# Kernel optimization log

Measured on AMD Instinct MI355X. Metric: run time of the kernel, lower is better.

Reference implementation:

```python
import jax, jax.numpy as jnp
import numpy as np

N, E, D, H, G = 40000, 640000, 128, 8, 64
DH = D // H
CUT = 8.0
LN2 = float(np.log(2.0))


def ssp(v):  # shifted softplus (SchNet activation)
    return jax.nn.softplus(v) - jnp.asarray(LN2, v.dtype)


def setup_inputs() -> dict:
    key = jax.random.key(0)
    ks = jax.random.split(key, 20)
    def lin(k, fi, fo):
        k1, k2 = jax.random.split(k)
        s = 1.0 / np.sqrt(fi)
        return (jax.random.uniform(k1, (fi, fo), jnp.float32, -s, s),
                jax.random.uniform(k2, (fo,), jnp.float32, -s, s))
    W_lin, b_lin = lin(ks[0], G, D)
    W_r1, b_r1 = lin(ks[1], G, D)
    W_r2, b_r2 = lin(ks[2], D, D)
    Wq, bq = lin(ks[3], D, D)
    Wk, bk = lin(ks[4], D, D)
    Wv, bv = lin(ks[5], D, D)
    Wo, bo = lin(ks[6], D, D)
    return {
        "x": jax.random.normal(ks[7], (N, D), jnp.float32),
        "t": jax.random.normal(ks[8], (N, D), jnp.float32),
        "f_ij": jax.random.uniform(ks[9], (E, G), jnp.float32),
        "r_ij": jax.random.uniform(ks[10], (E,), jnp.float32, 0.0, CUT),
        "src": jax.random.randint(ks[11], (E,), 0, N, jnp.int32),
        "dst": jax.random.randint(ks[12], (E,), 0, N, jnp.int32),
        "W_lin": W_lin, "b_lin": b_lin,
        "W_r1": W_r1, "b_r1": b_r1, "W_r2": W_r2, "b_r2": b_r2,
        "Wq": Wq, "bq": bq, "Wk": Wk, "bk": bk, "Wv": Wv, "bv": bv,
        "Wo": Wo, "bo": bo,
        "ln_g": jnp.ones((D,), jnp.float32),
        "ln_b": jnp.zeros((D,), jnp.float32),
    }


def reference(x, t, f_ij, r_ij, src, dst,
              W_lin, b_lin, W_r1, b_r1, W_r2, b_r2,
              Wq, bq, Wk, bk, Wv, bv, Wo, bo, ln_g, ln_b):
    # filter-generating network: linear branch + resnet branch (resnet=True)
    W = f_ij @ W_lin + b_lin + (ssp(f_ij @ W_r1 + b_r1) @ W_r2 + b_r2)  # [E, D]
    # cosine cutoff
    C = 0.5 * (jnp.cos(jnp.pi * r_ij / CUT) + 1.0) * (r_ij < CUT)  # [E]
    W = W * C[:, None]
    # time-conditioned node representation
    h = x + t  # [N, D]
    # ego attention: queries from destination node, keys/values from filtered messages
    q = (h @ Wq + bq).reshape(N, H, DH)
    m = h[src] * W  # filtered neighbor messages [E, D]
    k = (m @ Wk + bk).reshape(E, H, DH)
    v = (m @ Wv + bv).reshape(E, H, DH)
    scores = jnp.einsum('ehd,ehd->eh', q[dst], k) / np.sqrt(DH)  # [E, H]
    # per-destination segment softmax
    smax = jax.ops.segment_max(scores, dst, num_segments=N)  # [N, H]
    ex = jnp.exp(scores - smax[dst])
    den = jax.ops.segment_sum(ex, dst, num_segments=N)
    alpha = ex / (den[dst] + 1e-16)  # [E, H]
    agg = jax.ops.segment_sum(alpha[:, :, None] * v, dst, num_segments=N)  # [N, H, DH]
    vout = agg.reshape(N, D) @ Wo + bo
    # residual + post layer norm
    out = x + vout
    mu = jnp.mean(out, axis=-1, keepdims=True)
    var = jnp.var(out, axis=-1, keepdims=True)
    out = (out - mu) / jnp.sqrt(var + 1e-5) * ln_g + ln_b
    return out
```

## Files before the change

### kernel.cpp

```cpp
#include <hip/hip_runtime.h>

#define NN 40000
#define EE 640000
#define DD 128
#define HH 8
#define GG 64

typedef unsigned short u16;
typedef __attribute__((ext_vector_type(8))) short short8;
typedef __attribute__((ext_vector_type(4))) float f32x4;

__device__ __forceinline__ float bf2f(u16 u){ union{unsigned i;float f;}v; v.i=((unsigned)u)<<16; return v.f; }
__device__ __forceinline__ u16 f2bf(float f){ union{float f;unsigned i;}v; v.f=f; unsigned r=v.i+0x7fffu+((v.i>>16)&1u); return (u16)(r>>16); }
__device__ __forceinline__ float ssp_fast(float x){
  float t=fminf(x*1.4426950408889634f,126.0f);
  float p=__builtin_amdgcn_exp2f(t);
  return 0.6931471805599453f*(__builtin_amdgcn_logf(1.0f+p)-1.0f);
}

__device__ __forceinline__ bool bfmode(const void* lng){ return *(const unsigned*)lng == 0x3F803F80u; }
__device__ __forceinline__ float ldf(const void* p, int i, bool bf){
  return bf ? bf2f(((const u16*)p)[i]) : ((const float*)p)[i];
}
__device__ __forceinline__ u16 ldb(const void* p, int i, bool bf){
  return bf ? ((const u16*)p)[i] : f2bf(((const float*)p)[i]);
}

#define MFMA16(a,b,c) __builtin_amdgcn_mfma_f32_16x16x32_bf16((a),(b),(c),0,0,0)
__device__ __forceinline__ short8 frag16(const u16* p){ return *(const short8*)p; }

#define DPPADD(x,ctrl) do{ union{float f;int i;}_a,_b; _a.f=(x); \
  _b.i=__builtin_amdgcn_update_dpp(0,_a.i,(ctrl),0xF,0xF,true); (x)+=_b.f; }while(0)
__device__ __forceinline__ float red16(float x){
  DPPADD(x,0xB1); DPPADD(x,0x4E); DPPADD(x,0x124); DPPADD(x,0x128);
  return x;
}

__device__ __forceinline__ void bar_lgkm(){
  asm volatile("s_waitcnt lgkmcnt(0)\n\ts_barrier" ::: "memory");
}

__global__ __launch_bounds__(512) void k1_hq(const void* __restrict__ x, const void* __restrict__ t,
        const void* __restrict__ Wq, const void* __restrict__ bq, const void* __restrict__ lng,
        u16* __restrict__ h_out, u16* __restrict__ q_out){
  extern __shared__ u16 s1[];
  u16* wq = s1;
  u16* hb = wq+16384;
  float* bqf=(float*)(hb+8704);
  bool bf=bfmode(lng);
  {
    int cc=threadIdx.x&127, kg0=threadIdx.x>>7;
    for (int kg=kg0; kg<16; kg+=4){
      uint4 u; u16* tp=(u16*)&u;
      #pragma unroll
      for (int j=0;j<8;j++) tp[j]=ldb(Wq,(kg*8+j)*128+cc,bf);
      *(uint4*)&wq[(kg*128+cc)*8]=u;
    }
    if (threadIdx.x<128) bqf[threadIdx.x]=ldf(bq,threadIdx.x,bf);
  }
  int wave=threadIdx.x>>6, lane=threadIdx.x&63;
  int mb=wave>>1, nh=wave&1, lrow=lane&15, quad=lane>>4;
  int r0=blockIdx.x*64;
  #pragma unroll
  for (int i=0;i<2;i++){
    int idx=threadIdx.x+i*512;
    int row=idx>>4, part=idx&15;
    size_t g=(size_t)(r0+row)*128+part*8;
    uint4 u; u16* tp=(u16*)&u;
    if (bf){
      uint4 xv=*(const uint4*)((const u16*)x+g);
      uint4 tv=*(const uint4*)((const u16*)t+g);
      const u16* xp=(const u16*)&xv; const u16* tq=(const u16*)&tv;
      #pragma unroll
      for (int j=0;j<8;j++) tp[j]=f2bf(bf2f(xp[j])+bf2f(tq[j]));
    } else {
      const float* xp=(const float*)x+g; const float* tq=(const float*)t+g;
      float4 a0=*(const float4*)xp, a1=*(const float4*)(xp+4);
      float4 b0=*(const float4*)tq, b1=*(const float4*)(tq+4);
      float va[8]={a0.x+b0.x,a0.y+b0.y,a0.z+b0.z,a0.w+b0.w,
                   a1.x+b1.x,a1.y+b1.y,a1.z+b1.z,a1.w+b1.w};
      #pragma unroll
      for (int j=0;j<8;j++) tp[j]=f2bf(va[j]);
    }
    *(uint4*)&h_out[g]=u;
    *(uint4*)&hb[row*136+part*8]=u;
  }
  __syncthreads();
  short8 ma[4];
  const u16* mr=&hb[(mb*16+lrow)*136];
  #pragma unroll
  for (int ks=0;ks<4;ks++) ma[ks]=frag16(&mr[ks*32+quad*8]);
  #pragma unroll
  for (int nb=0;nb<4;nb++){
    int col=nh*64+nb*16+lrow;
    f32x4 acc={0.f,0.f,0.f,0.f};
    #pragma unroll
    for (int ks=0;ks<4;ks++) acc=MFMA16(ma[ks], frag16(&wq[((ks*4+quad)*128+col)*8]), acc);
    float bb=bqf[col];
    #pragma unroll
    for (int r=0;r<4;r++)
      q_out[(size_t)(r0+mb*16+quad*4+r)*128+col]=f2bf(acc[r]+bb);
  }
}

__global__ __launch_bounds__(256) void k_hist(const int* __restrict__ dst, int* __restrict__ counts){
  int e=blockIdx.x*256+threadIdx.x;
  atomicAdd(&counts[dst[e]],1);
}

__global__ __launch_bounds__(1024) void k_scan(const int* __restrict__ counts, int* __restrict__ row_start){
  __shared__ int part[1024];
  int tid=threadIdx.x;
  const int CH=(NN+1023)/1024;
  int base=tid*CH, s=0;
  for (int i=0;i<CH;i++){ int idx=base+i; if (idx<NN) s+=counts[idx]; }
  part[tid]=s; __syncthreads();
  for (int off=1;off<1024;off<<=1){
    int v=(tid>=off)?part[tid-off]:0;
    __syncthreads();
    part[tid]+=v;
    __syncthreads();
  }
  int run=part[tid]-s;
  for (int i=0;i<CH;i++){ int idx=base+i; if (idx<NN){ row_start[idx]=run; run+=counts[idx]; } }
  if (tid==1023) row_start[NN]=part[1023];
}

__global__ __launch_bounds__(256) void k_scatter(const int* __restrict__ dst, const int* __restrict__ row_start,
    int* __restrict__ cursor, int* __restrict__ edge_list){
  int e=blockIdx.x*256+threadIdx.x;
  int d=dst[e];
  int pos=row_start[d]+atomicAdd(&cursor[d],1);
  edge_list[pos]=e;
}

__global__ __launch_bounds__(512) void e_fused(
    const void* __restrict__ f_ij, const void* __restrict__ r_ij,
    const int* __restrict__ src, const int* __restrict__ dst,
    const void* __restrict__ W_lin, const void* __restrict__ b_lin,
    const void* __restrict__ W_r1, const void* __restrict__ b_r1,
    const void* __restrict__ W_r2, const void* __restrict__ b_r2,
    const void* __restrict__ Wk, const void* __restrict__ bk,
    const void* __restrict__ Wv, const void* __restrict__ bv,
    const void* __restrict__ lng,
    const u16* __restrict__ h_g, const u16* __restrict__ q_g,
    float* __restrict__ scores_out, u16* __restrict__ v_out)
{
  extern __shared__ u16 sm[];
  u16* wr1   = sm;
  u16* wlin  = wr1 + 8192;
  u16* wr2   = wlin + 8192;
  u16* wk    = wr2 + 16384;
  u16* ov    = wk + 16384;
  u16* f_lds = ov;
  u16* t_lds = ov + 4608;
  u16* m_lds = ov + 4608 + 8704;
  float* br1 = (float*)(sm + 71168);
  float* bl2 = br1 + 128;
  float* bkf = bl2 + 128;
  float* bvf = bkf + 128;
  bool bf = bfmode(lng);

  {
    int c=threadIdx.x&127, kg0=threadIdx.x>>7;
    for (int kg=kg0; kg<8; kg+=4){
      uint4 u; u16* tp=(u16*)&u;
      #pragma unroll
      for (int j=0;j<8;j++) tp[j]=ldb(W_r1,(kg*8+j)*128+c,bf);
      *(uint4*)&wr1[(kg*128+c)*8]=u;
      #pragma unroll
      for (int j=0;j<8;j++) tp[j]=ldb(W_lin,(kg*8+j)*128+c,bf);
      *(uint4*)&wlin[(kg*128+c)*8]=u;
    }
    for (int kg=kg0; kg<16; kg+=4){
      uint4 u; u16* tp=(u16*)&u;
      #pragma unroll
      for (int j=0;j<8;j++) tp[j]=ldb(W_r2,(kg*8+j)*128+c,bf);
      *(uint4*)&wr2[(kg*128+c)*8]=u;
      #pragma unroll
      for (int j=0;j<8;j++) tp[j]=ldb(Wk,(kg*8+j)*128+c,bf);
      *(uint4*)&wk[(kg*128+c)*8]=u;
      #pragma unroll
      for (int j=0;j<8;j++) tp[j]=ldb(Wv,(kg*8+j)*128+c,bf);
      *(uint4*)&ov[(kg*128+c)*8]=u;
    }
    if (threadIdx.x<128){
      br1[threadIdx.x]=ldf(b_r1,threadIdx.x,bf);
      bl2[threadIdx.x]=ldf(b_lin,threadIdx.x,bf)+ldf(b_r2,threadIdx.x,bf);
      bkf[threadIdx.x]=ldf(bk,threadIdx.x,bf);
      bvf[threadIdx.x]=ldf(bv,threadIdx.x,bf);
    }
  }
  __syncthreads();

  int wave=threadIdx.x>>6, lane=threadIdx.x&63;
  int mb=wave>>1, nh=wave&1, lrow=lane&15, quad=lane>>4;
  int erow0=mb*16+quad*4;
  int fedge=threadIdx.x>>3, fpart=threadIdx.x&7;
  const int NT=EE/64;

  short8 wvf[16];
  #pragma unroll
  for (int nb=0;nb<4;nb++){
    int col=nh*64+nb*16+lrow;
    #pragma unroll
    for (int ks=0;ks<4;ks++)
      wvf[nb*4+ks]=frag16(&ov[((ks*4+quad)*128+col)*8]);
  }
  __syncthreads();

  float4 fA, fB;
  int4 sv, dv;
  float rr0,rr1,rr2,rr3;
  u16 hc[4][4], qc[4][4];
  u16 hn[4][4], qn[4][4];
  float cc[4];

  auto LOAD_F=[&](int tt){
    if (bf){
      fA = *(const float4*)((const u16*)f_ij + (size_t)(tt*64+fedge)*64 + fpart*8);
    } else {
      const float* fp=(const float*)f_ij + (size_t)(tt*64+fedge)*64 + fpart*8;
      fA = *(const float4*)fp;
      fB = *(const float4*)(fp+4);
    }
  };
  auto WRITE_F=[&](){
    uint4 u;
    if (bf) u=*(uint4*)&fA;
    else {
      u16* tp=(u16*)&u;
      const float* a=(const float*)&fA;
      const float* b=(const float*)&fB;
      #pragma unroll
      for (int j=0;j<4;j++){ tp[j]=f2bf(a[j]); tp[4+j]=f2bf(b[j]); }
    }
    *(uint4*)&f_lds[fedge*72+fpart*8]=u;
  };
  auto LOAD_SDR=[&](int tt){
    sv=*(const int4*)&src[tt*64+erow0];
    dv=*(const int4*)&dst[tt*64+erow0];
    rr0=ldf(r_ij,tt*64+erow0+0,bf);
    rr1=ldf(r_ij,tt*64+erow0+1,bf);
    rr2=ldf(r_ij,tt*64+erow0+2,bf);
    rr3=ldf(r_ij,tt*64+erow0+3,bf);
  };
  auto LOAD_HQ=[&](u16 (&hd)[4][4], u16 (&qd)[4][4]){
    int sa[4]={sv.x,sv.y,sv.z,sv.w};
    int da[4]={dv.x,dv.y,dv.z,dv.w};
    #pragma unroll
    for (int nb=0;nb<4;nb++){
      int col=nh*64+nb*16+lrow;
      #pragma unroll
      for (int r=0;r<4;r++){
        hd[nb][r]=h_g[(size_t)sa[r]*128+col];
        qd[nb][r]=q_g[(size_t)da[r]*128+col];
      }
    }
  };
  auto CUTOFF=[&](){
    float ra[4]={rr0,rr1,rr2,rr3};
    #pragma unroll
    for (int r=0;r<4;r++)
      cc[r]=(ra[r]<8.0f)?0.5f*(__cosf(ra[r]*0.39269908169872414f)+1.0f):0.0f;
  };

  int tile=blockIdx.x;
  {
    LOAD_F(tile); LOAD_SDR(tile);
    WRITE_F();
    LOAD_HQ(hc,qc);
    CUTOFF();
  }
  __syncthreads();

  for (; tile<NT; tile+=gridDim.x){
    int tn=tile+gridDim.x; if (tn>=NT) tn=tile;

    const u16* fr=&f_lds[(mb*16+lrow)*72];
    short8 a0=frag16(&fr[quad*8]);
    short8 a1=frag16(&fr[32+quad*8]);

    LOAD_F(tn);
    LOAD_SDR(tn);

    #pragma unroll
    for (int nb=0;nb<4;nb++){
      int col=nh*64+nb*16+lrow;
      f32x4 acc={0.f,0.f,0.f,0.f};
      acc=MFMA16(a0, frag16(&wr1[(quad*128+col)*8]), acc);
      acc=MFMA16(a1, frag16(&wr1[((4+quad)*128+col)*8]), acc);
      float bb=br1[col];
      #pragma unroll
      for (int r=0;r<4;r++){
        int er=mb*16+quad*4+r;
        t_lds[er*136+col]=f2bf(ssp_fast(acc[r]+bb));
      }
    }
    bar_lgkm();

    WRITE_F();
    LOAD_HQ(hn,qn);

    short8 ta[4];
    const u16* tr=&t_lds[(mb*16+lrow)*136];
    #pragma unroll
    for (int ks=0;ks<4;ks++) ta[ks]=frag16(&tr[ks*32+quad*8]);
    #pragma unroll
    for (int nb=0;nb<4;nb++){
      int col=nh*64+nb*16+lrow;
      f32x4 acc={0.f,0.f,0.f,0.f};
      acc=MFMA16(a0, frag16(&wlin[(quad*128+col)*8]), acc);
      acc=MFMA16(a1, frag16(&wlin[((4+quad)*128+col)*8]), acc);
      #pragma unroll
      for (int ks=0;ks<4;ks++)
        acc=MFMA16(ta[ks], frag16(&wr2[((ks*4+quad)*128+col)*8]), acc);
      float bb=bl2[col];
      #pragma unroll
      for (int r=0;r<4;r++){
        int er=mb*16+quad*4+r;
        float u=(acc[r]+bb)*cc[r];
        m_lds[er*136+col]=f2bf(u*bf2f(hc[nb][r]));
      }
    }
    bar_lgkm();

    short8 ma[4];
    const u16* mr=&m_lds[(mb*16+lrow)*136];
    #pragma unroll
    for (int ks=0;ks<4;ks++) ma[ks]=frag16(&mr[ks*32+quad*8]);

    #pragma unroll
    for (int nb=0;nb<4;nb++){
      int col=nh*64+nb*16+lrow;
      f32x4 acc={0.f,0.f,0.f,0.f};
      #pragma unroll
      for (int ks=0;ks<4;ks++) acc=MFMA16(ma[ks], frag16(&wk[((ks*4+quad)*128+col)*8]), acc);
      float bb=bkf[col];
      float p[4];
      #pragma unroll
      for (int r=0;r<4;r++)
        p[r]=(acc[r]+bb)*bf2f(qc[nb][r]);
      #pragma unroll
      for (int r=0;r<4;r++) p[r]=red16(p[r]);
      if (lrow==0){
        int head=nh*4+nb;
        #pragma unroll
        for (int r=0;r<4;r++){
          int er=mb*16+quad*4+r;
          scores_out[(size_t)(tile*64+er)*8+head]=p[r]*0.25f;
        }
      }
      f32x4 av={0.f,0.f,0.f,0.f};
      #pragma unroll
      for (int ks=0;ks<4;ks++) av=MFMA16(ma[ks], wvf[nb*4+ks], av);
      float bb2=bvf[col];
      #pragma unroll
      for (int r=0;r<4;r++){
        int er=mb*16+quad*4+r;
        v_out[(size_t)(tile*64+er)*128+col]=f2bf(av[r]+bb2);
      }
    }

    #pragma unroll
    for (int nb=0;nb<4;nb++){
      #pragma unroll
      for (int r=0;r<4;r++){ hc[nb][r]=hn[nb][r]; qc[nb][r]=qn[nb][r]; }
    }
    CUTOFF();
  }
}

__global__ __launch_bounds__(256) void k3a_agg(
    const int* __restrict__ row_start, const int* __restrict__ edge_list,
    const float* __restrict__ scores, const u16* __restrict__ v_g,
    u16* __restrict__ agg_out)
{
  __shared__ int   el_s[2][128];
  __shared__ float al_s[2][128*8];
  __shared__ float mxden[2][16];
  int half=threadIdx.x>>7, tid=threadIdx.x&127;
  int n=blockIdx.x*2+half;
  int s0=row_start[n], s1=row_start[n+1], deg=s1-s0;
  int dc=min(deg,128);
  if (tid<dc) el_s[half][tid]=edge_list[s0+tid];
  __syncthreads();
  int h=tid>>4, j=tid&15;
  float mr=-1e30f, sr=0.f;
  for (int p=j;p<deg;p+=16){
    int e=(p<128)?el_s[half][p]:edge_list[s0+p];
    float sc=scores[(size_t)e*8+h];
    float mn=fmaxf(mr,sc);
    sr=sr*__expf(mr-mn)+__expf(sc-mn);
    mr=mn;
  }
  #pragma unroll
  for (int off=1;off<16;off<<=1){
    float m2=__shfl_xor(mr,off,64), s2=__shfl_xor(sr,off,64);
    float mn=fmaxf(mr,m2);
    sr=sr*__expf(mr-mn)+s2*__expf(m2-mn);
    mr=mn;
  }
  if (j==0){ mxden[half][h]=mr; mxden[half][8+h]=1.0f/(sr+1e-16f); }
  __syncthreads();
  {
    float mx=mxden[half][h], rd=mxden[half][8+h];
    for (int p=j;p<dc;p+=16){
      int e=el_s[half][p];
      al_s[half][p*8+h]=__expf(scores[(size_t)e*8+h]-mx)*rd;
    }
  }
  __syncthreads();
  int c=tid, hc=c>>4;
  float mxc=mxden[half][hc], rdc=mxden[half][8+hc];
  float agg=0.f;
  int p=0;
  for (; p+4<=dc; p+=4){
    int e0=el_s[half][p],   e1=el_s[half][p+1];
    int e2=el_s[half][p+2], e3=el_s[half][p+3];
    float a0=al_s[half][p*8+hc],     a1=al_s[half][(p+1)*8+hc];
    float a2=al_s[half][(p+2)*8+hc], a3=al_s[half][(p+3)*8+hc];
    agg += a0*bf2f(v_g[(size_t)e0*128+c]);
    agg += a1*bf2f(v_g[(size_t)e1*128+c]);
    agg += a2*bf2f(v_g[(size_t)e2*128+c]);
    agg += a3*bf2f(v_g[(size_t)e3*128+c]);
  }
  for (; p<dc; p++)
    agg += al_s[half][p*8+hc]*bf2f(v_g[(size_t)el_s[half][p]*128+c]);
  for (; p<deg; p++){
    int e=edge_list[s0+p];
    agg += __expf(scores[(size_t)e*8+hc]-mxc)*rdc*bf2f(v_g[(size_t)e*128+c]);
  }
  agg_out[(size_t)n*128+c]=f2bf(agg);
}

__global__ __launch_bounds__(512) void k3b_out(
    const u16* __restrict__ agg_g, const void* __restrict__ x_g,
    const void* __restrict__ Wo, const void* __restrict__ bo,
    const void* __restrict__ lng, const void* __restrict__ lnb,
    void* __restrict__ out)
{
  extern __shared__ u16 smb[];
  u16* wo = smb;
  u16* ag = wo+16384;
  float* bof=(float*)(ag+64*136);
  float* lgf=bof+128;
  float* lbf=lgf+128;
  float* rsum=lbf+128;
  float* rsq =rsum+128;
  bool bf=bfmode(lng);
  {
    int cc=threadIdx.x&127, kg0=threadIdx.x>>7;
    for (int kg=kg0; kg<16; kg+=4){
      uint4 u; u16* tp=(u16*)&u;
      #pragma unroll
      for (int jj=0;jj<8;jj++) tp[jj]=ldb(Wo,(kg*8+jj)*128+cc,bf);
      *(uint4*)&wo[(kg*128+cc)*8]=u;
    }
    if (threadIdx.x<128){
      bof[threadIdx.x]=ldf(bo,threadIdx.x,bf);
      lgf[threadIdx.x]=ldf(lng,threadIdx.x,bf);
      lbf[threadIdx.x]=ldf(lnb,threadIdx.x,bf);
    }
  }
  int wave=threadIdx.x>>6, lane=threadIdx.x&63;
  int mb=wave>>1, nh=wave&1, lrow=lane&15, quad=lane>>4;
  for (int tile=blockIdx.x; tile<NN/64; tile+=gridDim.x){
    int r0=tile*64;
    #pragma unroll
    for (int i=0;i<2;i++){
      int idx=threadIdx.x+i*512;
      int row=idx>>4, part=idx&15;
      uint4 d=*(const uint4*)&agg_g[(size_t)(r0+row)*128+part*8];
      *(uint4*)&ag[row*136+part*8]=d;
    }
    __syncthreads();
    short8 ma[4];
    const u16* mr=&ag[(mb*16+lrow)*136];
    #pragma unroll
    for (int ks=0;ks<4;ks++) ma[ks]=frag16(&mr[ks*32+quad*8]);
    float yv[4][4];
    float ps[4]={0,0,0,0}, pq[4]={0,0,0,0};
    #pragma unroll
    for (int nb=0;nb<4;nb++){
      int col=nh*64+nb*16+lrow;
      f32x4 acc={0.f,0.f,0.f,0.f};
      #pragma unroll
      for (int ks=0;ks<4;ks++) acc=MFMA16(ma[ks], frag16(&wo[((ks*4+quad)*128+col)*8]), acc);
      float bb=bof[col];
      #pragma unroll
      for (int r=0;r<4;r++){
        int row=r0+mb*16+quad*4+r;
        float y=ldf(x_g,row*128+col,bf)+acc[r]+bb;
        yv[nb][r]=y; ps[r]+=y; pq[r]+=y*y;
      }
    }
    #pragma unroll
    for (int r=0;r<4;r++){ ps[r]=red16(ps[r]); pq[r]=red16(pq[r]); }
    if (lrow==0){
      #pragma unroll
      for (int r=0;r<4;r++){
        int er=mb*16+quad*4+r;
        rsum[nh*64+er]=ps[r]; rsq[nh*64+er]=pq[r];
      }
    }
    __syncthreads();
    #pragma unroll
    for (int nb=0;nb<4;nb++){
      int col=nh*64+nb*16+lrow;
      float lg=lgf[col], lb=lbf[col];
      #pragma unroll
      for (int r=0;r<4;r++){
        int er=mb*16+quad*4+r;
        float ts=rsum[er]+rsum[64+er], tq=rsq[er]+rsq[64+er];
        float mu=ts*(1.f/128.f);
        float var=tq*(1.f/128.f)-mu*mu;
        float inv=rsqrtf(var+1e-5f);
        float o=(yv[nb][r]-mu)*inv*lg+lb;
        size_t oi=(size_t)(r0+er)*128+col;
        if (bf) ((u16*)out)[oi]=f2bf(o); else ((float*)out)[oi]=o;
      }
    }
    __syncthreads();
  }
}

extern "C" void kernel_launch(void* const* d_in, const int* in_sizes, int n_in,
                              void* d_out, int out_size, void* d_ws, size_t ws_size,
                              hipStream_t stream){
  (void)in_sizes; (void)n_in; (void)out_size; (void)ws_size;
  const void* x    =d_in[0];
  const void* t    =d_in[1];
  const void* f_ij =d_in[2];
  const void* r_ij =d_in[3];
  const int* src   =(const int*)d_in[4];
  const int* dst   =(const int*)d_in[5];
  const void* W_lin=d_in[6];
  const void* b_lin=d_in[7];
  const void* W_r1 =d_in[8];
  const void* b_r1 =d_in[9];
  const void* W_r2 =d_in[10];
  const void* b_r2 =d_in[11];
  const void* Wq   =d_in[12];
  const void* bq   =d_in[13];
  const void* Wk   =d_in[14];
  const void* bk   =d_in[15];
  const void* Wv   =d_in[16];
  const void* bv   =d_in[17];
  const void* Wo   =d_in[18];
  const void* bo   =d_in[19];
  const void* ln_g =d_in[20];
  const void* ln_b =d_in[21];

  char* ws=(char*)d_ws;
  size_t off=0;
  auto carve=[&](size_t bytes)->void*{ void* p=ws+off; off+=(bytes+255)&~(size_t)255; return p; };
  u16*   h_f     =(u16*)  carve((size_t)NN*DD*2);
  u16*   q_f     =(u16*)  carve((size_t)NN*DD*2);
  u16*   v_ws    =(u16*)  carve((size_t)EE*DD*2);
  float* sc_ws   =(float*)carve((size_t)EE*HH*4);
  u16*   agg_ws  =(u16*)  carve((size_t)NN*DD*2);
  int*   counts  =(int*)  carve((size_t)NN*4);
  int*   cursor  =(int*)  carve((size_t)NN*4);
  int*   row_start=(int*) carve((size_t)(NN+1)*4);
  int*   edge_list=(int*) carve((size_t)EE*4);

  hipMemsetAsync(counts,0,(size_t)NN*8,stream);

  const int K1_LDS=(16384+8704)*2 + 128*4;
  const int EF_LDS=71168*2 + 4*128*4;
  const int K3B_LDS=(16384+64*136)*2 + (128*3+128+128)*4;
  hipFuncSetAttribute((const void*)k1_hq,     hipFuncAttributeMaxDynamicSharedMemorySize, K1_LDS);
  hipFuncSetAttribute((const void*)e_fused,   hipFuncAttributeMaxDynamicSharedMemorySize, EF_LDS);
  hipFuncSetAttribute((const void*)k3b_out,   hipFuncAttributeMaxDynamicSharedMemorySize, K3B_LDS);

  k1_hq    <<<NN/64,  512, K1_LDS, stream>>>(x,t,Wq,bq,ln_g,h_f,q_f);
  k_hist   <<<EE/256, 256, 0, stream>>>(dst,counts);
  k_scan   <<<1,     1024, 0, stream>>>(counts,row_start);
  k_scatter<<<EE/256, 256, 0, stream>>>(dst,row_start,cursor,edge_list);
  e_fused  <<<256,    512, EF_LDS, stream>>>(f_ij,r_ij,src,dst,
                                             W_lin,b_lin,W_r1,b_r1,W_r2,b_r2,
                                             Wk,bk,Wv,bv,ln_g,h_f,q_f,sc_ws,v_ws);
  k3a_agg  <<<NN/2,   256, 0, stream>>>(row_start,edge_list,sc_ws,v_ws,agg_ws);
  k3b_out  <<<256,    512, K3B_LDS, stream>>>(agg_ws,x,Wo,bo,ln_g,ln_b,d_out);
}
```

Before: 729.3 us.

## Fuse histogram into edge kernel, rewrite aggregation per-wave, use packed bf16 converts

Result: slower. 898.8 us (+23.2%).

```diff
diff --git a/kernel.cpp b/kernel.cpp
--- a/kernel.cpp
+++ b/kernel.cpp
@@ -12,6 +12,11 @@
 
 __device__ __forceinline__ float bf2f(u16 u){ union{unsigned i;float f;}v; v.i=((unsigned)u)<<16; return v.f; }
 __device__ __forceinline__ u16 f2bf(float f){ union{float f;unsigned i;}v; v.f=f; unsigned r=v.i+0x7fffu+((v.i>>16)&1u); return (u16)(r>>16); }
+__device__ __forceinline__ unsigned cvt_pk_bf16(float lo, float hi){
+  unsigned r;
+  asm("v_cvt_pk_bf16_f32 %0, %1, %2" : "=v"(r) : "v"(lo), "v"(hi));
+  return r;
+}
 __device__ __forceinline__ float ssp_fast(float x){
   float t=fminf(x*1.4426950408889634f,126.0f);
   float p=__builtin_amdgcn_exp2f(t);
@@ -66,22 +71,23 @@
     int idx=threadIdx.x+i*512;
     int row=idx>>4, part=idx&15;
     size_t g=(size_t)(r0+row)*128+part*8;
-    uint4 u; u16* tp=(u16*)&u;
+    float s_[8];
     if (bf){
       uint4 xv=*(const uint4*)((const u16*)x+g);
       uint4 tv=*(const uint4*)((const u16*)t+g);
       const u16* xp=(const u16*)&xv; const u16* tq=(const u16*)&tv;
       #pragma unroll
-      for (int j=0;j<8;j++) tp[j]=f2bf(bf2f(xp[j])+bf2f(tq[j]));
+      for (int j=0;j<8;j++) s_[j]=bf2f(xp[j])+bf2f(tq[j]);
     } else {
       const float* xp=(const float*)x+g; const float* tq=(const float*)t+g;
       float4 a0=*(const float4*)xp, a1=*(const float4*)(xp+4);
       float4 b0=*(const float4*)tq, b1=*(const float4*)(tq+4);
-      float va[8]={a0.x+b0.x,a0.y+b0.y,a0.z+b0.z,a0.w+b0.w,
-                   a1.x+b1.x,a1.y+b1.y,a1.z+b1.z,a1.w+b1.w};
-      #pragma unroll
-      for (int j=0;j<8;j++) tp[j]=f2bf(va[j]);
-    }
+      s_[0]=a0.x+b0.x; s_[1]=a0.y+b0.y; s_[2]=a0.z+b0.z; s_[3]=a0.w+b0.w;
+      s_[4]=a1.x+b1.x; s_[5]=a1.y+b1.y; s_[6]=a1.z+b1.z; s_[7]=a1.w+b1.w;
+    }
+    uint4 u; unsigned* up=(unsigned*)&u;
+    up[0]=cvt_pk_bf16(s_[0],s_[1]); up[1]=cvt_pk_bf16(s_[2],s_[3]);
+    up[2]=cvt_pk_bf16(s_[4],s_[5]); up[3]=cvt_pk_bf16(s_[6],s_[7]);
     *(uint4*)&h_out[g]=u;
     *(uint4*)&hb[row*136+part*8]=u;
   }
@@ -97,15 +103,14 @@
     #pragma unroll
     for (int ks=0;ks<4;ks++) acc=MFMA16(ma[ks], frag16(&wq[((ks*4+quad)*128+col)*8]), acc);
     float bb=bqf[col];
-    #pragma unroll
-    for (int r=0;r<4;r++)
-      q_out[(size_t)(r0+mb*16+quad*4+r)*128+col]=f2bf(acc[r]+bb);
-  }
-}
-
-__global__ __launch_bounds__(256) void k_hist(const int* __restrict__ dst, int* __restrict__ counts){
-  int e=blockIdx.x*256+threadIdx.x;
-  atomicAdd(&counts[dst[e]],1);
+    unsigned p01=cvt_pk_bf16(acc[0]+bb,acc[1]+bb);
+    unsigned p23=cvt_pk_bf16(acc[2]+bb,acc[3]+bb);
+    unsigned base=(unsigned)(r0+mb*16+quad*4)*128+col;
+    q_out[base]      =(u16)p01;
+    q_out[base+128]  =(u16)(p01>>16);
+    q_out[base+256]  =(u16)p23;
+    q_out[base+384]  =(u16)(p23>>16);
+  }
 }
 
 __global__ __launch_bounds__(1024) void k_scan(const int* __restrict__ counts, int* __restrict__ row_start){
@@ -134,7 +139,7 @@
   edge_list[pos]=e;
 }
 
-__global__ __launch_bounds__(512) void e_fused(
+__global__ __launch_bounds__(512,2) void e_fused(
     const void* __restrict__ f_ij, const void* __restrict__ r_ij,
     const int* __restrict__ src, const int* __restrict__ dst,
     const void* __restrict__ W_lin, const void* __restrict__ b_lin,
@@ -144,7 +149,8 @@
     const void* __restrict__ Wv, const void* __restrict__ bv,
     const void* __restrict__ lng,
     const u16* __restrict__ h_g, const u16* __restrict__ q_g,
-    float* __restrict__ scores_out, u16* __restrict__ v_out)
+    float* __restrict__ scores_out, u16* __restrict__ v_out,
+    int* __restrict__ counts)
 {
   extern __shared__ u16 sm[];
   u16* wr1   = sm;
@@ -199,13 +205,18 @@
   int fedge=threadIdx.x>>3, fpart=threadIdx.x&7;
   const int NT=EE/64;
 
-  short8 wvf[16];
+  short8 wvf[16], wkf[16], wr2f[8];
   #pragma unroll
   for (int nb=0;nb<4;nb++){
     int col=nh*64+nb*16+lrow;
     #pragma unroll
-    for (int ks=0;ks<4;ks++)
+    for (int ks=0;ks<4;ks++){
       wvf[nb*4+ks]=frag16(&ov[((ks*4+quad)*128+col)*8]);
+      wkf[nb*4+ks]=frag16(&wk[((ks*4+quad)*128+col)*8]);
+    }
+    #pragma unroll
+    for (int ks=0;ks<2;ks++)
+      wr2f[nb*2+ks]=frag16(&wr2[((ks*4+quad)*128+col)*8]);
   }
   __syncthreads();
 
@@ -229,21 +240,32 @@
     uint4 u;
     if (bf) u=*(uint4*)&fA;
     else {
-      u16* tp=(u16*)&u;
+      unsigned* up=(unsigned*)&u;
       const float* a=(const float*)&fA;
       const float* b=(const float*)&fB;
-      #pragma unroll
-      for (int j=0;j<4;j++){ tp[j]=f2bf(a[j]); tp[4+j]=f2bf(b[j]); }
+      up[0]=cvt_pk_bf16(a[0],a[1]); up[1]=cvt_pk_bf16(a[2],a[3]);
+      up[2]=cvt_pk_bf16(b[0],b[1]); up[3]=cvt_pk_bf16(b[2],b[3]);
     }
     *(uint4*)&f_lds[fedge*72+fpart*8]=u;
   };
   auto LOAD_SDR=[&](int tt){
     sv=*(const int4*)&src[tt*64+erow0];
     dv=*(const int4*)&dst[tt*64+erow0];
-    rr0=ldf(r_ij,tt*64+erow0+0,bf);
-    rr1=ldf(r_ij,tt*64+erow0+1,bf);
-    rr2=ldf(r_ij,tt*64+erow0+2,bf);
-    rr3=ldf(r_ij,tt*64+erow0+3,bf);
+    if (bf){
+      rr0=bf2f(((const u16*)r_ij)[tt*64+erow0+0]);
+      rr1=bf2f(((const u16*)r_ij)[tt*64+erow0+1]);
+      rr2=bf2f(((const u16*)r_ij)[tt*64+erow0+2]);
+      rr3=bf2f(((const u16*)r_ij)[tt*64+erow0+3]);
+    } else {
+      float4 rv=*(const float4*)((const float*)r_ij + tt*64+erow0);
+      rr0=rv.x; rr1=rv.y; rr2=rv.z; rr3=rv.w;
+    }
+  };
+  auto HIST=[&](){
+    if (nh==0 && lrow==0){
+      atomicAdd(&counts[dv.x],1); atomicAdd(&counts[dv.y],1);
+      atomicAdd(&counts[dv.z],1); atomicAdd(&counts[dv.w],1);
+    }
   };
   auto LOAD_HQ=[&](u16 (&hd)[4][4], u16 (&qd)[4][4]){
     int sa[4]={sv.x,sv.y,sv.z,sv.w};
@@ -253,8 +275,8 @@
       int col=nh*64+nb*16+lrow;
       #pragma unroll
       for (int r=0;r<4;r++){
-        hd[nb][r]=h_g[(size_t)sa[r]*128+col];
-        qd[nb][r]=q_g[(size_t)da[r]*128+col];
+        hd[nb][r]=h_g[(unsigned)(sa[r]*128+col)];
+        qd[nb][r]=q_g[(unsigned)(da[r]*128+col)];
       }
     }
   };
@@ -262,7 +284,7 @@
     float ra[4]={rr0,rr1,rr2,rr3};
     #pragma unroll
     for (int r=0;r<4;r++)
-      cc[r]=(ra[r]<8.0f)?0.5f*(__cosf(ra[r]*0.39269908169872414f)+1.0f):0.0f;
+      cc[r]=(ra[r]<8.0f)?0.5f*(__builtin_amdgcn_cosf(ra[r]*0.0625f)+1.0f):0.0f;
   };
 
   int tile=blockIdx.x;
@@ -271,11 +293,12 @@
     WRITE_F();
     LOAD_HQ(hc,qc);
     CUTOFF();
+    HIST();
   }
   __syncthreads();
 
   for (; tile<NT; tile+=gridDim.x){
-    int tn=tile+gridDim.x; if (tn>=NT) tn=tile;
+    int tn=tile+gridDim.x; bool wrap=(tn>=NT); if (wrap) tn=tile;
 
     const u16* fr=&f_lds[(mb*16+lrow)*72];
     short8 a0=frag16(&fr[quad*8]);
@@ -283,6 +306,7 @@
 
     LOAD_F(tn);
     LOAD_SDR(tn);
+    if (!wrap) HIST();
 
     #pragma unroll
     for (int nb=0;nb<4;nb++){
@@ -291,11 +315,11 @@
       acc=MFMA16(a0, frag16(&wr1[(quad*128+col)*8]), acc);
       acc=MFMA16(a1, frag16(&wr1[((4+quad)*128+col)*8]), acc);
       float bb=br1[col];
-      #pragma unroll
-      for (int r=0;r<4;r++){
-        int er=mb*16+quad*4+r;
-        t_lds[er*136+col]=f2bf(ssp_fast(acc[r]+bb));
-      }
+      unsigned p01=cvt_pk_bf16(ssp_fast(acc[0]+bb),ssp_fast(acc[1]+bb));
+      unsigned p23=cvt_pk_bf16(ssp_fast(acc[2]+bb),ssp_fast(acc[3]+bb));
+      int a_=erow0*136+col;
+      t_lds[a_]    =(u16)p01;  t_lds[a_+136]=(u16)(p01>>16);
+      t_lds[a_+272]=(u16)p23;  t_lds[a_+408]=(u16)(p23>>16);
     }
     bar_lgkm();
 
@@ -313,15 +337,19 @@
       acc=MFMA16(a0, frag16(&wlin[(quad*128+col)*8]), acc);
       acc=MFMA16(a1, frag16(&wlin[((4+quad)*128+col)*8]), acc);
       #pragma unroll
-      for (int ks=0;ks<4;ks++)
-        acc=MFMA16(ta[ks], frag16(&wr2[((ks*4+quad)*128+col)*8]), acc);
+      for (int ks=0;ks<4;ks++){
+        short8 bfr=(ks<2)? wr2f[nb*2+ks] : frag16(&wr2[((ks*4+quad)*128+col)*8]);
+        acc=MFMA16(ta[ks], bfr, acc);
+      }
       float bb=bl2[col];
-      #pragma unroll
-      for (int r=0;r<4;r++){
-        int er=mb*16+quad*4+r;
-        float u=(acc[r]+bb)*cc[r];
-        m_lds[er*136+col]=f2bf(u*bf2f(hc[nb][r]));
-      }
+      float m0=(acc[0]+bb)*cc[0]*bf2f(hc[nb][0]);
+      float m1=(acc[1]+bb)*cc[1]*bf2f(hc[nb][1]);
+      float m2=(acc[2]+bb)*cc[2]*bf2f(hc[nb][2]);
+      float m3=(acc[3]+bb)*cc[3]*bf2f(hc[nb][3]);
+      unsigned p01=cvt_pk_bf16(m0,m1), p23=cvt_pk_bf16(m2,m3);
+      int a_=erow0*136+col;
+      m_lds[a_]    =(u16)p01;  m_lds[a_+136]=(u16)(p01>>16);
+      m_lds[a_+272]=(u16)p23;  m_lds[a_+408]=(u16)(p23>>16);
     }
     bar_lgkm();
 
@@ -335,7 +363,7 @@
       int col=nh*64+nb*16+lrow;
       f32x4 acc={0.f,0.f,0.f,0.f};
       #pragma unroll
-      for (int ks=0;ks<4;ks++) acc=MFMA16(ma[ks], frag16(&wk[((ks*4+quad)*128+col)*8]), acc);
+      for (int ks=0;ks<4;ks++) acc=MFMA16(ma[ks], wkf[nb*4+ks], acc);
       float bb=bkf[col];
       float p[4];
       #pragma unroll
@@ -345,21 +373,21 @@
       for (int r=0;r<4;r++) p[r]=red16(p[r]);
       if (lrow==0){
         int head=nh*4+nb;
-        #pragma unroll
-        for (int r=0;r<4;r++){
-          int er=mb*16+quad*4+r;
-          scores_out[(size_t)(tile*64+er)*8+head]=p[r]*0.25f;
-        }
+        unsigned sb=(unsigned)(tile*64+erow0)*8+head;
+        scores_out[sb]   =p[0]*0.25f;
+        scores_out[sb+8] =p[1]*0.25f;
+        scores_out[sb+16]=p[2]*0.25f;
+        scores_out[sb+24]=p[3]*0.25f;
       }
       f32x4 av={0.f,0.f,0.f,0.f};
       #pragma unroll
       for (int ks=0;ks<4;ks++) av=MFMA16(ma[ks], wvf[nb*4+ks], av);
       float bb2=bvf[col];
-      #pragma unroll
-      for (int r=0;r<4;r++){
-        int er=mb*16+quad*4+r;
-        v_out[(size_t)(tile*64+er)*128+col]=f2bf(av[r]+bb2);
-      }
+      unsigned p01=cvt_pk_bf16(av[0]+bb2,av[1]+bb2);
+      unsigned p23=cvt_pk_bf16(av[2]+bb2,av[3]+bb2);
+      unsigned vb=(unsigned)(tile*64+erow0)*128+col;
+      v_out[vb]    =(u16)p01;  v_out[vb+128]=(u16)(p01>>16);
+      v_out[vb+256]=(u16)p23;  v_out[vb+384]=(u16)(p23>>16);
     }
 
     #pragma unroll
@@ -376,62 +404,44 @@
     const float* __restrict__ scores, const u16* __restrict__ v_g,
     u16* __restrict__ agg_out)
 {
-  __shared__ int   el_s[2][128];
-  __shared__ float al_s[2][128*8];
-  __shared__ float mxden[2][16];
-  int half=threadIdx.x>>7, tid=threadIdx.x&127;
-  int n=blockIdx.x*2+half;
-  int s0=row_start[n], s1=row_start[n+1], deg=s1-s0;
-  int dc=min(deg,128);
-  if (tid<dc) el_s[half][tid]=edge_list[s0+tid];
-  __syncthreads();
-  int h=tid>>4, j=tid&15;
+  int wave=threadIdx.x>>6, lane=threadIdx.x&63;
+  int n=blockIdx.x*4+wave;
+  int s0=row_start[n], deg=row_start[n+1]-s0;
+  int h=lane>>3, j=lane&7;
   float mr=-1e30f, sr=0.f;
-  for (int p=j;p<deg;p+=16){
-    int e=(p<128)?el_s[half][p]:edge_list[s0+p];
-    float sc=scores[(size_t)e*8+h];
+  for (int p=j;p<deg;p+=8){
+    int e=edge_list[s0+p];
+    float sc=scores[(unsigned)(e*8+h)];
     float mn=fmaxf(mr,sc);
     sr=sr*__expf(mr-mn)+__expf(sc-mn);
     mr=mn;
   }
   #pragma unroll
-  for (int off=1;off<16;off<<=1){
+  for (int off=1;off<8;off<<=1){
     float m2=__shfl_xor(mr,off,64), s2=__shfl_xor(sr,off,64);
     float mn=fmaxf(mr,m2);
     sr=sr*__expf(mr-mn)+s2*__expf(m2-mn);
     mr=mn;
   }
-  if (j==0){ mxden[half][h]=mr; mxden[half][8+h]=1.0f/(sr+1e-16f); }
-  __syncthreads();
-  {
-    float mx=mxden[half][h], rd=mxden[half][8+h];
-    for (int p=j;p<dc;p+=16){
-      int e=el_s[half][p];
-      al_s[half][p*8+h]=__expf(scores[(size_t)e*8+h]-mx)*rd;
-    }
-  }
-  __syncthreads();
-  int c=tid, hc=c>>4;
-  float mxc=mxden[half][hc], rdc=mxden[half][8+hc];
-  float agg=0.f;
-  int p=0;
-  for (; p+4<=dc; p+=4){
-    int e0=el_s[half][p],   e1=el_s[half][p+1];
-    int e2=el_s[half][p+2], e3=el_s[half][p+3];
-    float a0=al_s[half][p*8+hc],     a1=al_s[half][(p+1)*8+hc];
-    float a2=al_s[half][(p+2)*8+hc], a3=al_s[half][(p+3)*8+hc];
-    agg += a0*bf2f(v_g[(size_t)e0*128+c]);
-    agg += a1*bf2f(v_g[(size_t)e1*128+c]);
-    agg += a2*bf2f(v_g[(size_t)e2*128+c]);
-    agg += a3*bf2f(v_g[(size_t)e3*128+c]);
-  }
-  for (; p<dc; p++)
-    agg += al_s[half][p*8+hc]*bf2f(v_g[(size_t)el_s[half][p]*128+c]);
-  for (; p<deg; p++){
+  float mx=mr, rd=1.0f/(sr+1e-16f);
+  int ecache=(lane<deg)?edge_list[s0+lane]:0;
+  float a0=0.f,a1=0.f;
+  int dcap=min(deg,64);
+  for (int p=0;p<dcap;p++){
+    int e=__builtin_amdgcn_readlane(ecache,p);
+    float al=__expf(scores[(unsigned)(e*8+h)]-mx);
+    unsigned vv=*(const unsigned*)&v_g[(unsigned)(e*128+lane*2)];
+    a0+=al*bf2f((u16)vv);
+    a1+=al*bf2f((u16)(vv>>16));
+  }
+  for (int p=64;p<deg;p++){
     int e=edge_list[s0+p];
-    agg += __expf(scores[(size_t)e*8+hc]-mxc)*rdc*bf2f(v_g[(size_t)e*128+c]);
-  }
-  agg_out[(size_t)n*128+c]=f2bf(agg);
+    float al=__expf(scores[(unsigned)(e*8+h)]-mx);
+    unsigned vv=*(const unsigned*)&v_g[(unsigned)(e*128+lane*2)];
+    a0+=al*bf2f((u16)vv);
+    a1+=al*bf2f((u16)(vv>>16));
+  }
+  *(unsigned*)&agg_out[(unsigned)(n*128+lane*2)]=cvt_pk_bf16(a0*rd,a1*rd);
 }
 
 __global__ __launch_bounds__(512) void k3b_out(
@@ -575,12 +585,11 @@
   hipFuncSetAttribute((const void*)k3b_out,   hipFuncAttributeMaxDynamicSharedMemorySize, K3B_LDS);
 
   k1_hq    <<<NN/64,  512, K1_LDS, stream>>>(x,t,Wq,bq,ln_g,h_f,q_f);
-  k_hist   <<<EE/256, 256, 0, stream>>>(dst,counts);
+  e_fused  <<<256,    512, EF_LDS, stream>>>(f_ij,r_ij,src,dst,
+                                             W_lin,b_lin,W_r1,b_r1,W_r2,b_r2,
+                                             Wk,bk,Wv,bv,ln_g,h_f,q_f,sc_ws,v_ws,counts);
   k_scan   <<<1,     1024, 0, stream>>>(counts,row_start);
   k_scatter<<<EE/256, 256, 0, stream>>>(dst,row_start,cursor,edge_list);
-  e_fused  <<<256,    512, EF_LDS, stream>>>(f_ij,r_ij,src,dst,
-                                             W_lin,b_lin,W_r1,b_r1,W_r2,b_r2,
-                                             Wk,bk,Wv,bv,ln_g,h_f,q_f,sc_ws,v_ws);
-  k3a_agg  <<<NN/2,   256, 0, stream>>>(row_start,edge_list,sc_ws,v_ws,agg_ws);
+  k3a_agg  <<<NN/4,   256, 0, stream>>>(row_start,edge_list,sc_ws,v_ws,agg_ws);
   k3b_out  <<<256,    512, K3B_LDS, stream>>>(agg_ws,x,Wo,bo,ln_g,ln_b,d_out);
 }
```
